# Performance work log

Measured on AMD Instinct MI355X. Metric: run time of the kernel, lower is better.

The kernel has to match this reference:

```python
import jax, jax.numpy as jnp
import numpy as np

B, CIN, H, W = 4, 64, 128, 128
COUT, K, S, P = 64, 3, 1, 1


def setup_inputs() -> dict:
    key = jax.random.key(0)
    k1, k2, k3, k4 = jax.random.split(key, 4)
    x = jax.random.normal(k1, (B, CIN, H, W), jnp.float32)
    # offset-predicting conv params (small scale so offsets stay in a sane range)
    offset_w = jax.random.normal(k2, (2 * K * K, CIN, K, K), jnp.float32) * 0.01
    offset_b = jnp.zeros((2 * K * K,), jnp.float32)
    # deformable conv params
    fan_in = CIN * K * K
    deform_w = jax.random.normal(k3, (COUT, CIN, K, K), jnp.float32) / np.sqrt(fan_in).astype(np.float32)
    deform_b = jax.random.normal(k4, (COUT,), jnp.float32) * 0.01
    return {"x": x, "offset_w": offset_w, "offset_b": offset_b,
            "deform_w": deform_w, "deform_b": deform_b}


def _conv2d(x, w, b, stride, pad):
    y = jax.lax.conv_general_dilated(
        x, w, window_strides=(stride, stride),
        padding=[(pad, pad), (pad, pad)],
        dimension_numbers=("NCHW", "OIHW", "NCHW"))
    return y + b[None, :, None, None]


def _deform_conv2d(x, offset, w, b, stride, pad):
    Bn, C, Hi, Wi = x.shape
    O, _, Kh, Kw = w.shape
    KK = Kh * Kw
    Ho = (Hi + 2 * pad - Kh) // stride + 1
    Wo = (Wi + 2 * pad - Kw) // stride + 1
    # offset layout (torchvision/mmcv): [B, KK, 2, Ho, Wo] with (dy, dx)
    off = offset.reshape(Bn, KK, 2, Ho, Wo)
    dy, dx = off[:, :, 0], off[:, :, 1]
    ky, kx = jnp.meshgrid(jnp.arange(Kh), jnp.arange(Kw), indexing="ij")
    ky = ky.reshape(-1).astype(x.dtype)  # [KK]
    kx = kx.reshape(-1).astype(x.dtype)
    hgrid = (jnp.arange(Ho) * stride - pad).astype(x.dtype)  # [Ho]
    wgrid = (jnp.arange(Wo) * stride - pad).astype(x.dtype)  # [Wo]
    # fractional sampling coords [B, KK, Ho, Wo]
    ys = hgrid[None, None, :, None] + ky[None, :, None, None] + dy
    xs = wgrid[None, None, None, :] + kx[None, :, None, None] + dx
    y0 = jnp.floor(ys)
    x0 = jnp.floor(xs)
    ly = (ys - y0)[:, None]  # [B,1,KK,Ho,Wo] for channel broadcast
    lx = (xs - x0)[:, None]
    y0i = y0.astype(jnp.int32)
    x0i = x0.astype(jnp.int32)

    def samp(yi, xi):
        valid = (yi >= 0) & (yi < Hi) & (xi >= 0) & (xi < Wi)
        yc = jnp.clip(yi, 0, Hi - 1)
        xc = jnp.clip(xi, 0, Wi - 1)
        # per-batch gather -> [B, C, KK, Ho, Wo]
        v = jax.vmap(lambda im, yy, xx: im[:, yy, xx])(x, yc, xc)
        return v * valid[:, None].astype(x.dtype)

    v00 = samp(y0i, x0i)
    v01 = samp(y0i, x0i + 1)
    v10 = samp(y0i + 1, x0i)
    v11 = samp(y0i + 1, x0i + 1)
    sampled = (v00 * (1 - ly) * (1 - lx) + v01 * (1 - ly) * lx
               + v10 * ly * (1 - lx) + v11 * ly * lx)  # [B,C,KK,Ho,Wo]
    out = jnp.einsum("bckhw,ock->bohw", sampled, w.reshape(O, C, KK))
    return out + b[None, :, None, None]


def reference(x, offset_w, offset_b, deform_w, deform_b):
    offset = _conv2d(x, offset_w, offset_b, S, P)
    return _deform_conv2d(x, offset, deform_w, deform_b, S, P)
```

## Files before the change

### kernel.cpp

```cpp
#include <hip/hip_runtime.h>
#include <hip/hip_bf16.h>

#define B_    4
#define CIN_  64
#define H_    128
#define W_    128
#define COUT_ 64
#define KK_   9
#define OFFC_ 18
#define HW_   (H_*W_)
#define TILE_ 64

typedef short bf8  __attribute__((ext_vector_type(8)));
typedef float f32x4 __attribute__((ext_vector_type(4)));

__device__ inline short f2bf(float f) {
    union { __hip_bfloat16 h; short s; } u; u.h = __float2bfloat16(f); return u.s;
}
__device__ inline float bf2f(short s) {
    union { unsigned u; float f; } v; v.u = ((unsigned)(unsigned short)s) << 16; return v.f;
}

__global__ __launch_bounds__(256) void prep_all(
    const float* __restrict__ x,
    const float* __restrict__ ow, const float* __restrict__ dw,
    short* __restrict__ xt, short* __restrict__ dwbf, short* __restrict__ owbf)
{
    const int tid = threadIdx.x;
    const int bid = blockIdx.x;
    if (bid < 1024) {
        const int b  = bid >> 8;
        const int pb = bid & 255;
        const int p  = tid & 63;
        const int g  = tid >> 6;
        const int pix = pb * 64 + p;
        const float* src = x + ((size_t)b * CIN_ + g * 16) * HW_ + pix;
        short vals[16];
        #pragma unroll
        for (int j = 0; j < 16; ++j) vals[j] = f2bf(src[(size_t)j * HW_]);
        short* dst = xt + ((size_t)b * HW_ + pix) * 64 + g * 16;
        *(bf8*)dst       = *(bf8*)&vals[0];
        *(bf8*)(dst + 8) = *(bf8*)&vals[8];
    } else {
        const int idx = (bid - 1024) * 256 + tid;
        {
            const int k = idx / (COUT_ * CIN_);
            const int r = idx % (COUT_ * CIN_);
            const int o = r >> 6, c = r & 63;
            dwbf[idx] = f2bf(dw[(o * CIN_ + c) * KK_ + k]);
        }
        if (idx < KK_ * 32 * CIN_) {
            const int k = idx / (32 * CIN_);
            const int r = idx % (32 * CIN_);
            const int co = r >> 6, c = r & 63;
            owbf[idx] = f2bf(co < OFFC_ ? ow[(co * CIN_ + c) * KK_ + k] : 0.0f);
        }
    }
}

__global__ __launch_bounds__(256, 4) void fused_deform_mfma(
    const short* __restrict__ xt,
    const short* __restrict__ owbf,
    const float* __restrict__ obias,
    const short* __restrict__ dwbf,
    const float* __restrict__ dbias,
    float* __restrict__ out)
{
    __shared__ union {
        short xtl[3 * 66 * 64];
        short smp[2 * 64 * 64];
    } u;
    __shared__ float offs[OFFC_ * TILE_];

    const int lin  = blockIdx.x;
    const int nid  = (lin & 7) * 128 + (lin >> 3);
    const int b    = nid >> 8;
    const int tile = nid & 255;

    const int tid = threadIdx.x;
    const int pixbase = tile * TILE_;
    const int ho    = pixbase >> 7;
    const int wbase = pixbase & (W_ - 1);
    const int lane  = tid & 63;
    const int wv    = tid >> 6;
    const int arow  = lane & 15;
    const int kseg  = lane >> 4;

    const short* xbt = xt + (size_t)b * HW_ * 64;

    for (int base = 0; base < 3 * 66 * 8; base += 256) {
        const int idx = base + tid;
        if (idx < 3 * 66 * 8) {
            const int cc = idx & 7;
            const int qy = idx >> 3;
            const int y  = qy / 66;
            const int q  = qy - y * 66;
            const int gy = ho + y - 1;
            const int gx = wbase + q - 1;
            bf8 v;
            if (gy >= 0 && gy < H_ && gx >= 0 && gx < W_) {
                v = *(const bf8*)&xbt[(size_t)(gy * W_ + gx) * 64 + cc * 8];
            } else {
                #pragma unroll
                for (int j = 0; j < 8; ++j) v[j] = 0;
            }
            *(bf8*)&u.xtl[(y * 66 + q) * 64 + ((cc ^ (q & 7)) << 3)] = v;
        }
    }
    __syncthreads();

    {
        const int m = wv & 1;
        const int h = wv >> 1;
        f32x4 acca[2];
        acca[0] = (f32x4)0.f; acca[1] = (f32x4)0.f;
        for (int t = 0; t < KK_; ++t) {
            const int ky = t / 3, kx = t % 3;
            #pragma unroll
            for (int kc = 0; kc < 2; ++kc) {
                const int cbase = kc * 32 + kseg * 8;
                const bf8 afrag = *(const bf8*)&owbf[(t * 32 + m * 16 + arow) * 64 + cbase];
                const int cchunk = cbase >> 3;
                #pragma unroll
                for (int nt = 0; nt < 2; ++nt) {
                    const int pp = h * 32 + nt * 16 + arow;
                    const int q = pp + kx;
                    const bf8 bfrag = *(const bf8*)&u.xtl[(ky * 66 + q) * 64 + ((cchunk ^ (q & 7)) << 3)];
                    acca[nt] = __builtin_amdgcn_mfma_f32_16x16x32_bf16(afrag, bfrag, acca[nt], 0, 0, 0);
                }
            }
        }
        #pragma unroll
        for (int nt = 0; nt < 2; ++nt) {
            #pragma unroll
            for (int r = 0; r < 4; ++r) {
                const int co = m * 16 + kseg * 4 + r;
                if (co < OFFC_) {
                    const int pp = h * 32 + nt * 16 + arow;
                    offs[co * TILE_ + pp] = acca[nt][r] + obias[co];
                }
            }
        }
    }
    __syncthreads();

    const int pix16 = lane >> 2;
    const int sub   = lane & 3;
    const int p     = wv * 16 + pix16;
    const int wo    = wbase + p;

    bf8 r00a, r00b, r01a, r01b, r10a, r10b, r11a, r11b;
    float pm00, pm01, pm10, pm11;

    auto loadB = [&](int t) {
        const int ky = t / 3, kx = t % 3;
        const float dy = offs[(2 * t + 0) * TILE_ + p];
        const float dx = offs[(2 * t + 1) * TILE_ + p];
        const float ys = (float)(ho + ky - 1) + dy;
        const float xs = (float)(wo + kx - 1) + dx;
        const float y0f = floorf(ys), x0f = floorf(xs);
        const float ly = ys - y0f, lx = xs - x0f;
        const int y0 = (int)y0f, x0 = (int)x0f;
        const int y1 = y0 + 1,   x1 = x0 + 1;
        const bool y0v = (y0 >= 0) & (y0 < H_);
        const bool y1v = (y1 >= 0) & (y1 < H_);
        const bool x0v = (x0 >= 0) & (x0 < W_);
        const bool x1v = (x1 >= 0) & (x1 < W_);
        pm00 = (y0v & x0v) ? (1.f - ly) * (1.f - lx) : 0.f;
        pm01 = (y0v & x1v) ? (1.f - ly) * lx         : 0.f;
        pm10 = (y1v & x0v) ? ly * (1.f - lx)         : 0.f;
        pm11 = (y1v & x1v) ? ly * lx                 : 0.f;
        const int y0c = min(max(y0, 0), H_ - 1);
        const int y1c = min(max(y1, 0), H_ - 1);
        const int x0c = min(max(x0, 0), W_ - 1);
        const int x1c = min(max(x1, 0), W_ - 1);
        const short* c00 = xbt + (size_t)(y0c * W_ + x0c) * 64 + sub * 8;
        const short* c01 = xbt + (size_t)(y0c * W_ + x1c) * 64 + sub * 8;
        const short* c10 = xbt + (size_t)(y1c * W_ + x0c) * 64 + sub * 8;
        const short* c11 = xbt + (size_t)(y1c * W_ + x1c) * 64 + sub * 8;
        r00a = *(const bf8*)(c00); r00b = *(const bf8*)(c00 + 32);
        r01a = *(const bf8*)(c01); r01b = *(const bf8*)(c01 + 32);
        r10a = *(const bf8*)(c10); r10b = *(const bf8*)(c10 + 32);
        r11a = *(const bf8*)(c11); r11b = *(const bf8*)(c11 + 32);
    };

    auto combineWrite = [&](int dstbuf) {
        bf8 va, vb;
        #pragma unroll
        for (int j = 0; j < 8; ++j) {
            const float sa = pm00 * bf2f(r00a[j]) + pm01 * bf2f(r01a[j])
                           + pm10 * bf2f(r10a[j]) + pm11 * bf2f(r11a[j]);
            const float sb = pm00 * bf2f(r00b[j]) + pm01 * bf2f(r01b[j])
                           + pm10 * bf2f(r10b[j]) + pm11 * bf2f(r11b[j]);
            va[j] = f2bf(sa);
            vb[j] = f2bf(sb);
        }
        const int cA = sub;
        const int cB = sub + 4;
        *(bf8*)&u.smp[dstbuf * 4096 + p * 64 + ((cA ^ (p & 7)) << 3)] = va;
        *(bf8*)&u.smp[dstbuf * 4096 + p * 64 + ((cB ^ (p & 7)) << 3)] = vb;
    };

    f32x4 accb[4];
    #pragma unroll
    for (int nt = 0; nt < 4; ++nt) accb[nt] = (f32x4)0.f;

    int buf = 0;
    loadB(0);
    combineWrite(0);
    __syncthreads();
    for (int t = 0; t < KK_; ++t) {
        if (t < KK_ - 1) loadB(t + 1);
        #pragma unroll
        for (int kc = 0; kc < 2; ++kc) {
            const int cbase = kc * 32 + kseg * 8;
            const bf8 afrag = *(const bf8*)&dwbf[(t * 64 + wv * 16 + arow) * 64 + cbase];
            const int cchunk = cbase >> 3;
            #pragma unroll
            for (int nt = 0; nt < 4; ++nt) {
                const int pp = nt * 16 + arow;
                const bf8 bfrag = *(const bf8*)&u.smp[buf * 4096 + pp * 64 + ((cchunk ^ (pp & 7)) << 3)];
                accb[nt] = __builtin_amdgcn_mfma_f32_16x16x32_bf16(afrag, bfrag, accb[nt], 0, 0, 0);
            }
        }
        if (t < KK_ - 1) combineWrite(buf ^ 1);
        __syncthreads();
        buf ^= 1;
    }

    float* ob = out + (size_t)b * COUT_ * HW_ + pixbase;
    #pragma unroll
    for (int nt = 0; nt < 4; ++nt) {
        const int pp = nt * 16 + arow;
        #pragma unroll
        for (int r = 0; r < 4; ++r) {
            const int o = wv * 16 + kseg * 4 + r;
            ob[(size_t)o * HW_ + pp] = accb[nt][r] + dbias[o];
        }
    }
}

extern "C" void kernel_launch(void* const* d_in, const int* in_sizes, int n_in,
                              void* d_out, int out_size, void* d_ws, size_t ws_size,
                              hipStream_t stream) {
    const float* x        = (const float*)d_in[0];
    const float* offset_w = (const float*)d_in[1];
    const float* offset_b = (const float*)d_in[2];
    const float* deform_w = (const float*)d_in[3];
    const float* deform_b = (const float*)d_in[4];
    float* out = (float*)d_out;

    short* dwbf = (short*)d_ws;
    short* owbf = (short*)((char*)d_ws + 73728);
    short* xt   = (short*)((char*)d_ws + 110592);

    prep_all<<<1024 + 144, 256, 0, stream>>>(x, offset_w, deform_w, xt, dwbf, owbf);

    fused_deform_mfma<<<1024, 256, 0, stream>>>(xt, owbf, offset_b, dwbf, deform_b, out);
}
```

Before: 48.13 us.

## Read offset-conv operands straight from global memory and drop the LDS halo tile

The offset-predicting conv no longer stages a 3x66x64 halo tile of x in shared memory. Each lane loads its B fragment directly from global/L2, and the work is remapped so each wave owns 16 pixels and computes both 16-row output-channel halves. This removes one LDS fill, one barrier and the union, so LDS per block shrinks and launch bounds go up to 5 blocks per CU. It also skips the barrier after the last tap. The cost is redundant global loads of overlapping neighbourhoods across the nine taps, which now rely on cache hits instead of shared memory.

Result: slower. 61.10 us (+26.9%).

```diff
diff --git a/kernel.cpp b/kernel.cpp
--- a/kernel.cpp
+++ b/kernel.cpp
@@ -58,7 +58,7 @@
     }
 }
 
-__global__ __launch_bounds__(256, 4) void fused_deform_mfma(
+__global__ __launch_bounds__(256, 5) void fused_deform_mfma(
     const short* __restrict__ xt,
     const short* __restrict__ owbf,
     const float* __restrict__ obias,
@@ -66,10 +66,7 @@
     const float* __restrict__ dbias,
     float* __restrict__ out)
 {
-    __shared__ union {
-        short xtl[3 * 66 * 64];
-        short smp[2 * 64 * 64];
-    } u;
+    __shared__ short smp[2 * 64 * 64];
     __shared__ float offs[OFFC_ * TILE_];
 
     const int lin  = blockIdx.x;
@@ -88,57 +85,35 @@
 
     const short* xbt = xt + (size_t)b * HW_ * 64;
 
-    for (int base = 0; base < 3 * 66 * 8; base += 256) {
-        const int idx = base + tid;
-        if (idx < 3 * 66 * 8) {
-            const int cc = idx & 7;
-            const int qy = idx >> 3;
-            const int y  = qy / 66;
-            const int q  = qy - y * 66;
-            const int gy = ho + y - 1;
-            const int gx = wbase + q - 1;
-            bf8 v;
-            if (gy >= 0 && gy < H_ && gx >= 0 && gx < W_) {
-                v = *(const bf8*)&xbt[(size_t)(gy * W_ + gx) * 64 + cc * 8];
-            } else {
-                #pragma unroll
-                for (int j = 0; j < 8; ++j) v[j] = 0;
-            }
-            *(bf8*)&u.xtl[(y * 66 + q) * 64 + ((cc ^ (q & 7)) << 3)] = v;
-        }
-    }
-    __syncthreads();
-
     {
-        const int m = wv & 1;
-        const int h = wv >> 1;
+        const int px = wv * 16 + arow;
+        const int gxbase = wbase + px - 1;
         f32x4 acca[2];
         acca[0] = (f32x4)0.f; acca[1] = (f32x4)0.f;
         for (int t = 0; t < KK_; ++t) {
             const int ky = t / 3, kx = t % 3;
+            const int gy = ho + ky - 1;
+            const int gx = gxbase + kx;
+            const bool v = (gy >= 0) & (gy < H_) & (gx >= 0) & (gx < W_);
+            const short* bp = xbt + (size_t)(gy * W_ + gx) * 64 + kseg * 8;
             #pragma unroll
             for (int kc = 0; kc < 2; ++kc) {
-                const int cbase = kc * 32 + kseg * 8;
-                const bf8 afrag = *(const bf8*)&owbf[(t * 32 + m * 16 + arow) * 64 + cbase];
-                const int cchunk = cbase >> 3;
-                #pragma unroll
-                for (int nt = 0; nt < 2; ++nt) {
-                    const int pp = h * 32 + nt * 16 + arow;
-                    const int q = pp + kx;
-                    const bf8 bfrag = *(const bf8*)&u.xtl[(ky * 66 + q) * 64 + ((cchunk ^ (q & 7)) << 3)];
-                    acca[nt] = __builtin_amdgcn_mfma_f32_16x16x32_bf16(afrag, bfrag, acca[nt], 0, 0, 0);
-                }
+                bf8 bfrag;
+                if (v) bfrag = *(const bf8*)(bp + kc * 32);
+                else   bfrag = (bf8)0;
+                const short* ap = owbf + (size_t)(t * 32 + arow) * 64 + kc * 32 + kseg * 8;
+                const bf8 a0 = *(const bf8*)(ap);
+                const bf8 a1 = *(const bf8*)(ap + 16 * 64);
+                acca[0] = __builtin_amdgcn_mfma_f32_16x16x32_bf16(a0, bfrag, acca[0], 0, 0, 0);
+                acca[1] = __builtin_amdgcn_mfma_f32_16x16x32_bf16(a1, bfrag, acca[1], 0, 0, 0);
             }
         }
         #pragma unroll
-        for (int nt = 0; nt < 2; ++nt) {
+        for (int m = 0; m < 2; ++m) {
             #pragma unroll
             for (int r = 0; r < 4; ++r) {
                 const int co = m * 16 + kseg * 4 + r;
-                if (co < OFFC_) {
-                    const int pp = h * 32 + nt * 16 + arow;
-                    offs[co * TILE_ + pp] = acca[nt][r] + obias[co];
-                }
+                if (co < OFFC_) offs[co * TILE_ + px] = acca[m][r] + obias[co];
             }
         }
     }
@@ -197,8 +172,8 @@
         }
         const int cA = sub;
         const int cB = sub + 4;
-        *(bf8*)&u.smp[dstbuf * 4096 + p * 64 + ((cA ^ (p & 7)) << 3)] = va;
-        *(bf8*)&u.smp[dstbuf * 4096 + p * 64 + ((cB ^ (p & 7)) << 3)] = vb;
+        *(bf8*)&smp[dstbuf * 4096 + p * 64 + ((cA ^ (p & 7)) << 3)] = va;
+        *(bf8*)&smp[dstbuf * 4096 + p * 64 + ((cB ^ (p & 7)) << 3)] = vb;
     };
 
     f32x4 accb[4];
@@ -219,12 +194,14 @@
             #pragma unroll
             for (int nt = 0; nt < 4; ++nt) {
                 const int pp = nt * 16 + arow;
-                const bf8 bfrag = *(const bf8*)&u.smp[buf * 4096 + pp * 64 + ((cchunk ^ (pp & 7)) << 3)];
+                const bf8 bfrag = *(const bf8*)&smp[buf * 4096 + pp * 64 + ((cchunk ^ (pp & 7)) << 3)];
                 accb[nt] = __builtin_amdgcn_mfma_f32_16x16x32_bf16(afrag, bfrag, accb[nt], 0, 0, 0);
             }
         }
-        if (t < KK_ - 1) combineWrite(buf ^ 1);
-        __syncthreads();
+        if (t < KK_ - 1) {
+            combineWrite(buf ^ 1);
+            __syncthreads();
+        }
         buf ^= 1;
     }
 
```
